# Performance work log

Hardware: AMD Instinct MI355X
Metric: run time of the kernel (lower is better)

## Reference

```python
import jax, jax.numpy as jnp
import numpy as np

WB = 8   # weight bit width (signed int8, power-of-two scale)
AB = 8   # activation bit width (uint8, power-of-two scale)
BB = 8   # bias bit width

# (name, c_in, c_out, kernel) for every QuantConv2d in order
_CFG = [("1", 3, 32, 3), ("2", 32, 16, 3), ("31", 16, 16, 1), ("32", 16, 32, 3),
        ("33", 32, 32, 1), ("34", 32, 64, 3), ("41", 64, 32, 1), ("42", 32, 64, 3),
        ("43", 64, 32, 1), ("44", 32, 64, 3), ("45", 64, 32, 1), ("46", 32, 64, 3)]
_POOL_AFTER = {"1", "2", "34"}  # MaxPool2d(2,2) follows these blocks


def _ste_round(x):
    # straight-through rounding (Brevitas-style fake quant)
    return x + jax.lax.stop_gradient(jnp.round(x) - x)


def _p2_scale(maxv, levels):
    # power-of-two (fixed point) per-tensor scale covering maxv with `levels` steps
    maxv = jnp.maximum(jax.lax.stop_gradient(maxv), 1e-8)
    return 2.0 ** jnp.ceil(jnp.log2(maxv / levels))


def quant_int(x, bw):
    # signed symmetric fixed-point fake quant (Int8WeightPerTensorFixedPoint style)
    n = 2.0 ** (bw - 1) - 1.0
    s = _p2_scale(jnp.max(jnp.abs(x)), n)
    return jnp.clip(_ste_round(x / s), -n - 1.0, n) * s


def quant_uint(x, bw):
    # unsigned fixed-point fake quant (Uint8ActPerTensorFixedPoint style)
    n = 2.0 ** bw - 1.0
    s = _p2_scale(jnp.max(x), n)
    return jnp.clip(_ste_round(x / s), 0.0, n) * s


def _conv(x, w, pad):
    return jax.lax.conv_general_dilated(
        x, w, window_strides=(1, 1), padding=[(pad, pad), (pad, pad)],
        dimension_numbers=("NCHW", "OIHW", "NCHW"))


def _maxpool2(x):
    return jax.lax.reduce_window(x, -jnp.inf, jax.lax.max,
                                 (1, 1, 2, 2), (1, 1, 2, 2), "VALID")


def _forward(x, p):
    # QuantIdentity on input (uint8 fixed point)
    x = quant_uint(x, AB)
    for n, ci, co, k in _CFG:
        pad = (k - 1) // 2
        y = _conv(x, quant_int(p["w" + n], WB), pad)               # quantized conv, no bias
        # BatchNorm2dToQuantScaleBias: per-channel affine with quantized scale/bias
        y = (y * quant_int(p["sg" + n], WB)[None, :, None, None]
             + quant_int(p["sb" + n], BB)[None, :, None, None])
        x = quant_uint(jax.nn.relu(y), AB)                          # QuantReLU
        if n in _POOL_AFTER:
            x = _maxpool2(x)
    # TruncAvgPool2d(28,28) over the remaining 28x28 map + RoundTo8bit requant
    x = quant_uint(jnp.mean(x, axis=(2, 3)), 8)                     # [B, 64]
    h = x @ quant_int(p["fw1"], WB).T + quant_int(p["fb1"], BB)     # linear51
    h = quant_uint(jax.nn.relu(h), AB)                              # relu5
    return h @ quant_int(p["fw2"], WB).T + quant_int(p["fb2"], BB)  # linear52


def setup_inputs() -> dict:
    key = jax.random.key(0)
    ks = iter(jax.random.split(key, 64))
    inp = {"x": jax.random.uniform(next(ks), (16, 3, 224, 224), jnp.float32)}
    for n, ci, co, k in _CFG:
        inp["w" + n] = jax.random.normal(next(ks), (co, ci, k, k), jnp.float32) * 0.1
        inp["sg" + n] = jax.random.uniform(next(ks), (co,), jnp.float32, 0.5, 1.5)
        inp["sb" + n] = jax.random.normal(next(ks), (co,), jnp.float32) * 0.1
    inp["fw1"] = jax.random.normal(next(ks), (16, 64), jnp.float32) * 0.1
    inp["fb1"] = jax.random.normal(next(ks), (16,), jnp.float32) * 0.1
    inp["fw2"] = jax.random.normal(next(ks), (10, 16), jnp.float32) * 0.1
    inp["fb2"] = jax.random.normal(next(ks), (10,), jnp.float32) * 0.1
    return inp


def reference(x, w1, sg1, sb1, w2, sg2, sb2, w31, sg31, sb31, w32, sg32, sb32,
              w33, sg33, sb33, w34, sg34, sb34, w41, sg41, sb41, w42, sg42, sb42,
              w43, sg43, sb43, w44, sg44, sb44, w45, sg45, sb45, w46, sg46, sb46,
              fw1, fb1, fw2, fb2):
    p = dict(locals())
    x = p.pop("x")
    return _forward(x, p)
```

## Files before the change

### kernel.cpp

```cpp
#include <hip/hip_runtime.h>
#include <math.h>

#define NL 12

typedef short v8s __attribute__((ext_vector_type(8)));
typedef float v4f __attribute__((ext_vector_type(4)));

struct PrepArgs {
  const float* in[40];
  void* out[40];
  int n[40];
  int mode[40];
  int tc[40];
  int ci[40], kk[40], kp[40], co[40];
};

__device__ inline float p2_scale_f(float maxv, float levels) {
  float r = __fdiv_rn(fmaxf(maxv, 1e-8f), levels);
  unsigned b = __float_as_uint(r);
  unsigned e = (b >> 23) & 0xffu;
  e += (b & 0x7fffffu) ? 1u : 0u;
  return __uint_as_float(e << 23);
}

__device__ inline float p2_inv(float s) {
  return __uint_as_float((254u << 23) - __float_as_uint(s));
}

__device__ inline float block_reduce_max256(float v) {
  __shared__ float sm[4];
  #pragma unroll
  for (int off = 32; off; off >>= 1) v = fmaxf(v, __shfl_down(v, off));
  if ((threadIdx.x & 63) == 0) sm[threadIdx.x >> 6] = v;
  __syncthreads();
  if (threadIdx.x == 0) v = fmaxf(fmaxf(sm[0], sm[1]), fmaxf(sm[2], sm[3]));
  return v;
}

__device__ inline void slot_max_update(float* slot, float v) {
  volatile unsigned int* su = (volatile unsigned int*)slot;
  unsigned int bits = __float_as_uint(v);
  if (bits > *su) atomicMax((unsigned int*)slot, bits);
}

__device__ inline short ibf16(float v) {
  return (short)(__float_as_uint(v) >> 16);
}

__global__ void prep_kernel(PrepArgs a, float* wslot,
                            const float* __restrict__ x, int nx, float* slot0) {
  if (blockIdx.x >= 40) {
    const float4* xv = (const float4*)x;
    const int nv = nx >> 2;
    float m0 = 0.f, m1 = 0.f, m2 = 0.f, m3 = 0.f;
    for (int i = (blockIdx.x - 40) * 256 + threadIdx.x; i < nv;
         i += (gridDim.x - 40) * 256) {
      float4 v = xv[i];
      m0 = fmaxf(m0, v.x); m1 = fmaxf(m1, v.y);
      m2 = fmaxf(m2, v.z); m3 = fmaxf(m3, v.w);
    }
    float m = fmaxf(fmaxf(m0, m1), fmaxf(m2, m3));
    float bm = block_reduce_max256(m);
    if (threadIdx.x == 0) slot_max_update(slot0, bm);
    return;
  }
  __shared__ float ssc;
  const int t = blockIdx.x;
  const float* in = a.in[t];
  const int n = a.n[t], mode = a.mode[t];
  float m = 0.f;
  if (mode == 2) {
    const float4* in4 = (const float4*)in;
    const int n4 = n >> 2;
    for (int i = threadIdx.x; i < n4; i += 256) {
      float4 v = in4[i];
      m = fmaxf(m, fmaxf(fmaxf(fabsf(v.x), fabsf(v.y)),
                         fmaxf(fabsf(v.z), fabsf(v.w))));
    }
  } else {
    for (int i = threadIdx.x; i < n; i += 256) m = fmaxf(m, fabsf(in[i]));
  }
  float bm = block_reduce_max256(m);
  if (threadIdx.x == 0) {
    ssc = p2_scale_f(bm, 127.0f);
    if (mode == 2) wslot[t] = ssc;
  }
  __syncthreads();
  const float s = ssc;
  if (mode == 2) {
    ushort* o = (ushort*)a.out[t];
    const int CI = a.ci[t], KK = a.kk[t], KP = a.kp[t], CO = a.co[t];
    const int KT = CI * KK;
    for (int i = threadIdx.x; i < CO * KP; i += 256) {
      int co = i / KP, k = i % KP;
      ushort v = 0;
      if (k < KT) {
        int khkw = k / CI, ci = k % CI;
        float q = rintf(__fdiv_rn(in[(co * CI + ci) * KK + khkw], s));
        q = fminf(fmaxf(q, -128.f), 127.f);
        v = (ushort)(__float_as_uint(q) >> 16);
      }
      o[i] = v;
    }
  } else {
    float* o = (float*)a.out[t];
    const int tc = a.tc[t];
    const int nw = (mode == 1) ? n / tc : 1;
    for (int i = threadIdx.x; i < n; i += 256) {
      float q = rintf(__fdiv_rn(in[i], s));
      q = fminf(fmaxf(q, -128.f), 127.f);
      float v = __fmul_rn(q, s);
      if (mode == 1) o[(i % nw) * tc + i / nw] = v;
      else o[i] = v;
    }
  }
}


template <int CI, int H, int CO, bool K3, bool POOL, int CSPLIT>
__global__ __launch_bounds__(256)
void conv_mfma(const float* __restrict__ in, const short* __restrict__ wt,
               const float* __restrict__ sg, const float* __restrict__ sb,
               float* __restrict__ out, const float* __restrict__ slot_in,
               const float* __restrict__ wslotp, float* slot_out) {
  constexpr int W = H;
  constexpr int KT = (K3 ? 9 : 1) * CI;
  constexpr int SLABS = (KT + 31) / 32;
  constexpr int KP = SLABS * 32;
  constexpr int COT = CO / (16 * CSPLIT);
  constexpr int HO = POOL ? H / 2 : H;
  constexpr int WO = POOL ? W / 2 : W;

  const int lane = threadIdx.x & 63, widx = threadIdx.x >> 6;
  const int quad = lane >> 4, col = lane & 15;
  const float s_in = p2_scale_f(slot_in[0], 255.0f);
  const float inv = p2_inv(s_in);
  const float S = __fmul_rn(s_in, wslotp[0]);
  const int wv = blockIdx.x * 4 + widx;
  const int mt = wv / CSPLIT, ct = wv % CSPLIT;

  int n, h, w, ph = 0, pw = 0;
  if constexpr (POOL) {
    constexpr int PB = (HO / 2) * (WO / 2);
    n = mt / PB; int r = mt % PB;
    ph = r / (WO / 2); pw = r % (WO / 2);
    h = 4 * ph + (col >> 2); w = 4 * pw + (col & 3);
  } else {
    int p = mt * 16 + col;
    n = p / (H * W); int r = p % (H * W);
    h = r / W; w = r % W;
  }
  const float* ibase = in + (size_t)n * H * W * CI;

  float4 fa[SLABS], fb[SLABS];
  bool vm[SLABS];
  #pragma unroll
  for (int slab = 0; slab < SLABS; slab++) {
    const int kbase = slab * 32 + quad * 8;
    const float* ap;
    if constexpr (K3) {
      const int khkw = min(kbase / CI, 8);
      const int cib = kbase % CI;
      const int kh = khkw / 3, kw = khkw - kh * 3;
      const int hh = h + kh - 1, ww = w + kw - 1;
      vm[slab] = (hh >= 0) && (hh < H) && (ww >= 0) && (ww < W);
      const int hc = min(max(hh, 0), H - 1), wc = min(max(ww, 0), W - 1);
      ap = ibase + (size_t)(hc * W + wc) * CI + cib;
    } else {
      vm[slab] = true;
      ap = ibase + (size_t)(h * W + w) * CI + (kbase % CI);
    }
    fa[slab] = ((const float4*)ap)[0];
    fb[slab] = ((const float4*)ap)[1];
  }

  v4f acc[COT];
  #pragma unroll
  for (int c = 0; c < COT; c++) acc[c] = (v4f){0.f, 0.f, 0.f, 0.f};

  #pragma unroll
  for (int slab = 0; slab < SLABS; slab++) {
    const int kbase = slab * 32 + quad * 8;
    float ff[8] = {fa[slab].x, fa[slab].y, fa[slab].z, fa[slab].w,
                   fb[slab].x, fb[slab].y, fb[slab].z, fb[slab].w};
    v8s a;
    #pragma unroll
    for (int j = 0; j < 8; j++) {
      float q = rintf(__fmul_rn(ff[j], inv));
      a[j] = vm[slab] ? ibf16(q) : (short)0;
    }
    #pragma unroll
    for (int c = 0; c < COT; c++) {
      v8s b = *(const v8s*)(wt + (size_t)((ct * COT + c) * 16 + col) * KP + kbase);
      acc[c] = __builtin_amdgcn_mfma_f32_16x16x32_bf16(a, b, acc[c], 0, 0, 0);
    }
  }

  float zmax = 0.f;
  #pragma unroll
  for (int c = 0; c < COT; c++) {
    const int cog = (ct * COT + c) * 16 + col;
    const float g = sg[cog], bb = sb[cog];
    float z[4];
    #pragma unroll
    for (int r2 = 0; r2 < 4; r2++) {
      float t = __fmul_rn(acc[c][r2], S);
      z[r2] = fmaxf(__fadd_rn(__fmul_rn(t, g), bb), 0.f);
    }
    if constexpr (POOL) {
      float h0 = fmaxf(z[0], z[1]), h1 = fmaxf(z[2], z[3]);
      float o0 = fmaxf(h0, __shfl_xor(h0, 16));
      float o1 = fmaxf(h1, __shfl_xor(h1, 16));
      zmax = fmaxf(zmax, fmaxf(o0, o1));
      if (!(quad & 1)) {
        int oh = 2 * ph + (quad >> 1), ow = 2 * pw;
        float* op = out + ((size_t)((n * HO + oh) * WO + ow)) * CO + cog;
        op[0] = o0; op[CO] = o1;
      }
    } else {
      const int pbase = mt * 16 + quad * 4;
      #pragma unroll
      for (int r2 = 0; r2 < 4; r2++) {
        out[(size_t)(pbase + r2) * CO + cog] = z[r2];
        zmax = fmaxf(zmax, z[r2]);
      }
    }
  }
  float bm = block_reduce_max256(zmax);
  if (threadIdx.x == 0) slot_max_update(slot_out, bm);
}

__global__ __launch_bounds__(256)
void conv1_mfma(const float* __restrict__ x, const short* __restrict__ wt,
                const float* __restrict__ sg, const float* __restrict__ sb,
                float* __restrict__ out, const float* __restrict__ slot_in,
                const float* __restrict__ wslotp, float* slot_out) {
  const int lane = threadIdx.x & 63, widx = threadIdx.x >> 6;
  const int quad = lane >> 4, col = lane & 15;
  const float s_in = p2_scale_f(slot_in[0], 255.0f);
  const float inv = p2_inv(s_in);
  const float S = __fmul_rn(s_in, wslotp[0]);
  const int wv = blockIdx.x * 4 + widx;
  const int n = wv / 3136, r = wv % 3136;
  const int ph = r / 56, pw = r % 56;
  const int h = 4 * ph + (col >> 2), w = 4 * pw + (col & 3);

  float fv[8];
  bool vm[8];
  #pragma unroll
  for (int j = 0; j < 8; j++) {
    int k = quad * 8 + j;
    int kc = min(k, 26);
    int khkw = kc / 3, ci = kc - khkw * 3;
    int kh = khkw / 3, kw = khkw - kh * 3;
    int hh = h + kh - 1, ww = w + kw - 1;
    vm[j] = (hh >= 0) && (hh < 224) && (ww >= 0) && (ww < 224);
    int hc = min(max(hh, 0), 223), wc = min(max(ww, 0), 223);
    fv[j] = x[((n * 3 + ci) * 224 + hc) * 224 + wc];
  }
  v8s a;
  #pragma unroll
  for (int j = 0; j < 8; j++) {
    float q = rintf(__fmul_rn(fv[j], inv));
    a[j] = vm[j] ? ibf16(q) : (short)0;
  }
  v4f acc[2];
  acc[0] = (v4f){0.f, 0.f, 0.f, 0.f};
  acc[1] = acc[0];
  #pragma unroll
  for (int c = 0; c < 2; c++) {
    v8s b = *(const v8s*)(wt + (size_t)(c * 16 + col) * 32 + quad * 8);
    acc[c] = __builtin_amdgcn_mfma_f32_16x16x32_bf16(a, b, acc[c], 0, 0, 0);
  }
  float zmax = 0.f;
  #pragma unroll
  for (int c = 0; c < 2; c++) {
    const int cog = c * 16 + col;
    const float g = sg[cog], bb = sb[cog];
    float z[4];
    #pragma unroll
    for (int r2 = 0; r2 < 4; r2++) {
      float t = __fmul_rn(acc[c][r2], S);
      z[r2] = fmaxf(__fadd_rn(__fmul_rn(t, g), bb), 0.f);
    }
    float h0 = fmaxf(z[0], z[1]), h1 = fmaxf(z[2], z[3]);
    float o0 = fmaxf(h0, __shfl_xor(h0, 16));
    float o1 = fmaxf(h1, __shfl_xor(h1, 16));
    zmax = fmaxf(zmax, fmaxf(o0, o1));
    if (!(quad & 1)) {
      int oh = 2 * ph + (quad >> 1), ow = 2 * pw;
      float* op = out + ((size_t)((n * 112 + oh) * 112 + ow)) * 32 + cog;
      op[0] = o0; op[32] = o1;
    }
  }
  float bm = block_reduce_max256(zmax);
  if (threadIdx.x == 0) slot_max_update(slot_out, bm);
}

__global__ void avgpool_kernel(const float* __restrict__ in, float* __restrict__ out,
                               const float* __restrict__ slot_in, float* slot_out) {
  __shared__ float red[1024];
  const float s = p2_scale_f(slot_in[0], 255.0f);
  const float inv = p2_inv(s);
  const int nn = blockIdx.x, co = threadIdx.x & 63, part = threadIdx.x >> 6;
  const float* p = in + (size_t)nn * 784 * 64;
  float sum = 0.f;
  for (int i = part * 49; i < part * 49 + 49; i++)
    sum += __fmul_rn(rintf(__fmul_rn(p[i * 64 + co], inv)), s);
  red[threadIdx.x] = sum;
  __syncthreads();
  if (threadIdx.x < 64) {
    float tot = 0.f;
    #pragma unroll
    for (int k2 = 0; k2 < 16; k2++) tot += red[k2 * 64 + co];
    float m = __fdiv_rn(tot, 784.0f);
    out[nn * 64 + co] = m;
    slot_max_update(slot_out, m);
  }
}

__global__ void tail_kernel(const float* __restrict__ pooled,
                            const float* __restrict__ fw1, const float* __restrict__ fb1,
                            const float* __restrict__ fw2, const float* __restrict__ fb2,
                            const float* __restrict__ slot_in, float* __restrict__ out) {
  __shared__ float xq[1024];
  __shared__ float hq[256];
  __shared__ float s2s;
  const int t = threadIdx.x;
  const float s = p2_scale_f(slot_in[0], 255.0f);
  const float inv = p2_inv(s);
  for (int i = t; i < 1024; i += 256)
    xq[i] = __fmul_rn(rintf(__fmul_rn(pooled[i], inv)), s);
  __syncthreads();
  const int n = t >> 4, j = t & 15;
  float acc = 0.f;
  #pragma unroll 8
  for (int k = 0; k < 64; k++) acc += xq[n * 64 + k] * fw1[k * 16 + j];
  float z = fmaxf(__fadd_rn(acc, fb1[j]), 0.f);
  float bm = block_reduce_max256(z);
  if (t == 0) s2s = p2_scale_f(bm, 255.0f);
  __syncthreads();
  const float s2 = s2s, inv2 = p2_inv(s2);
  hq[t] = __fmul_rn(rintf(__fmul_rn(z, inv2)), s2);
  __syncthreads();
  if (t < 160) {
    const int n2 = t / 10, j2 = t % 10;
    float a2 = 0.f;
    #pragma unroll
    for (int k = 0; k < 16; k++) a2 += hq[n2 * 16 + k] * fw2[k * 10 + j2];
    out[t] = __fadd_rn(a2, fb2[j2]);
  }
}

extern "C" void kernel_launch(void* const* d_in, const int* in_sizes, int n_in,
                              void* d_out, int out_size, void* d_ws, size_t ws_size,
                              hipStream_t stream) {
  static const int h_ci[NL] = {3, 32, 16, 16, 32, 32, 64, 32, 64, 32, 64, 32};
  static const int h_co[NL] = {32, 16, 16, 32, 32, 64, 32, 64, 32, 64, 32, 64};
  static const int h_kk[NL] = {9, 9, 1, 9, 1, 9, 1, 9, 1, 9, 1, 9};
  static const int h_kp[NL] = {32, 288, 32, 160, 32, 288, 64, 288, 64, 288, 64, 288};

  float* ws = (float*)d_ws;
  float* slots = ws;
  float* wslot = ws + 16;
  size_t off = 32;

  short* wq[NL];
  for (int l = 0; l < NL; l++) {
    wq[l] = (short*)(ws + off);
    off += (size_t)(h_co[l] * h_kp[l] + 1) / 2;
  }
  float* sgq[NL]; float* sbq[NL];
  for (int l = 0; l < NL; l++) { sgq[l] = ws + off; off += 64; }
  for (int l = 0; l < NL; l++) { sbq[l] = ws + off; off += 64; }
  float* fw1q = ws + off; off += 1024;
  float* fb1q = ws + off; off += 16;
  float* fw2q = ws + off; off += 160;
  float* fb2q = ws + off; off += 16;
  float* A = ws + off; off += 6422528;
  float* B = ws + off; off += 1605632;
  float* P = ws + off; off += 1024;

  PrepArgs pa;
  for (int l = 0; l < NL; l++) {
    pa.in[l] = (const float*)d_in[1 + 3 * l]; pa.out[l] = (void*)wq[l];
    pa.n[l] = h_co[l] * h_ci[l] * h_kk[l];
    pa.mode[l] = 2; pa.tc[l] = 0;
    pa.ci[l] = h_ci[l]; pa.kk[l] = h_kk[l]; pa.kp[l] = h_kp[l]; pa.co[l] = h_co[l];
    pa.in[12 + l] = (const float*)d_in[2 + 3 * l]; pa.out[12 + l] = (void*)sgq[l];
    pa.n[12 + l] = h_co[l]; pa.mode[12 + l] = 0; pa.tc[12 + l] = 0;
    pa.ci[12 + l] = pa.kk[12 + l] = pa.kp[12 + l] = pa.co[12 + l] = 0;
    pa.in[24 + l] = (const float*)d_in[3 + 3 * l]; pa.out[24 + l] = (void*)sbq[l];
    pa.n[24 + l] = h_co[l]; pa.mode[24 + l] = 0; pa.tc[24 + l] = 0;
    pa.ci[24 + l] = pa.kk[24 + l] = pa.kp[24 + l] = pa.co[24 + l] = 0;
  }
  pa.in[36] = (const float*)d_in[37]; pa.out[36] = (void*)fw1q;
  pa.n[36] = 1024; pa.mode[36] = 1; pa.tc[36] = 16;
  pa.ci[36] = pa.kk[36] = pa.kp[36] = pa.co[36] = 0;
  pa.in[37] = (const float*)d_in[38]; pa.out[37] = (void*)fb1q;
  pa.n[37] = 16; pa.mode[37] = 0; pa.tc[37] = 0;
  pa.ci[37] = pa.kk[37] = pa.kp[37] = pa.co[37] = 0;
  pa.in[38] = (const float*)d_in[39]; pa.out[38] = (void*)fw2q;
  pa.n[38] = 160; pa.mode[38] = 1; pa.tc[38] = 10;
  pa.ci[38] = pa.kk[38] = pa.kp[38] = pa.co[38] = 0;
  pa.in[39] = (const float*)d_in[40]; pa.out[39] = (void*)fb2q;
  pa.n[39] = 10; pa.mode[39] = 0; pa.tc[39] = 0;
  pa.ci[39] = pa.kk[39] = pa.kp[39] = pa.co[39] = 0;

  const float* x = (const float*)d_in[0];
  const int nx = 16 * 3 * 224 * 224;

  hipMemsetAsync(slots, 0, 16 * sizeof(float), stream);
  prep_kernel<<<40 + 294, 256, 0, stream>>>(pa, wslot, x, nx, slots + 0);

  conv1_mfma<<<12544, 256, 0, stream>>>(x, wq[0], sgq[0], sbq[0], A,
                                        slots + 0, wslot + 0, slots + 1);
  conv_mfma<32, 112, 16, true, true, 1><<<3136, 256, 0, stream>>>(
      A, wq[1], sgq[1], sbq[1], B, slots + 1, wslot + 1, slots + 2);
  conv_mfma<16, 56, 16, false, false, 1><<<784, 256, 0, stream>>>(
      B, wq[2], sgq[2], sbq[2], A, slots + 2, wslot + 2, slots + 3);
  conv_mfma<16, 56, 32, true, false, 2><<<1568, 256, 0, stream>>>(
      A, wq[3], sgq[3], sbq[3], B, slots + 3, wslot + 3, slots + 4);
  conv_mfma<32, 56, 32, false, false, 2><<<1568, 256, 0, stream>>>(
      B, wq[4], sgq[4], sbq[4], A, slots + 4, wslot + 4, slots + 5);
  conv_mfma<32, 56, 64, true, true, 2><<<1568, 256, 0, stream>>>(
      A, wq[5], sgq[5], sbq[5], B, slots + 5, wslot + 5, slots + 6);
  conv_mfma<64, 28, 32, false, false, 2><<<392, 256, 0, stream>>>(
      B, wq[6], sgq[6], sbq[6], A, slots + 6, wslot + 6, slots + 7);
  conv_mfma<32, 28, 64, true, false, 2><<<392, 256, 0, stream>>>(
      A, wq[7], sgq[7], sbq[7], B, slots + 7, wslot + 7, slots + 8);
  conv_mfma<64, 28, 32, false, false, 2><<<392, 256, 0, stream>>>(
      B, wq[8], sgq[8], sbq[8], A, slots + 8, wslot + 8, slots + 9);
  conv_mfma<32, 28, 64, true, false, 2><<<392, 256, 0, stream>>>(
      A, wq[9], sgq[9], sbq[9], B, slots + 9, wslot + 9, slots + 10);
  conv_mfma<64, 28, 32, false, false, 2><<<392, 256, 0, stream>>>(
      B, wq[10], sgq[10], sbq[10], A, slots + 10, wslot + 10, slots + 11);
  conv_mfma<32, 28, 64, true, false, 2><<<392, 256, 0, stream>>>(
      A, wq[11], sgq[11], sbq[11], B, slots + 11, wslot + 11, slots + 12);

  avgpool_kernel<<<16, 1024, 0, stream>>>(B, P, slots + 12, slots + 13);
  tail_kernel<<<1, 256, 0, stream>>>(P, fw1q, fb1q, fw2q, fb2q, slots + 13,
                                     (float*)d_out);
}
```

Measured before the change: 383.2 us.

## Pre-quantize input into channel-interleaved bf16 layout for conv1 tap loads

Adds a separate kernel that quantizes the input image once into an NHWC4 bf16 buffer. conv1 then loads one 8-byte vector per 3x3 tap instead of eight scattered fp32 loads from the three channel planes. The conv1 weights are repacked to 64-wide K so the taps map onto two MFMAs. This trades an extra pass over the input and an extra launch for cheaper, coalesced conv1 gathers and no per-element quantization in the conv.

```diff
diff --git a/kernel.cpp b/kernel.cpp
--- a/kernel.cpp
+++ b/kernel.cpp
@@ -69,7 +69,7 @@
   const float* in = a.in[t];
   const int n = a.n[t], mode = a.mode[t];
   float m = 0.f;
-  if (mode == 2) {
+  if (mode >= 2) {
     const float4* in4 = (const float4*)in;
     const int n4 = n >> 2;
     for (int i = threadIdx.x; i < n4; i += 256) {
@@ -83,11 +83,24 @@
   float bm = block_reduce_max256(m);
   if (threadIdx.x == 0) {
     ssc = p2_scale_f(bm, 127.0f);
-    if (mode == 2) wslot[t] = ssc;
+    if (mode >= 2) wslot[t] = ssc;
   }
   __syncthreads();
   const float s = ssc;
-  if (mode == 2) {
+  if (mode == 3) {
+    ushort* o = (ushort*)a.out[t];
+    for (int i = threadIdx.x; i < 32 * 64; i += 256) {
+      int co = i >> 6, k = i & 63;
+      int khkw = k >> 2, ci = k & 3;
+      ushort v = 0;
+      if (khkw < 9 && ci < 3) {
+        float q = rintf(__fdiv_rn(in[(co * 3 + ci) * 9 + khkw], s));
+        q = fminf(fmaxf(q, -128.f), 127.f);
+        v = (ushort)(__float_as_uint(q) >> 16);
+      }
+      o[i] = v;
+    }
+  } else if (mode == 2) {
     ushort* o = (ushort*)a.out[t];
     const int CI = a.ci[t], KK = a.kk[t], KP = a.kp[t], CO = a.co[t];
     const int KT = CI * KK;
@@ -114,6 +127,28 @@
       else o[i] = v;
     }
   }
+}
+
+__global__ void quantx_kernel(const float* __restrict__ x, ushort* __restrict__ xt,
+                              const float* __restrict__ slot_in) {
+  const float s = p2_scale_f(slot_in[0], 255.0f);
+  const float inv = p2_inv(s);
+  const int nh = blockIdx.x;
+  const int w = threadIdx.x;
+  if (w >= 224) return;
+  const int n = nh / 224;
+  const float* base = x + (size_t)n * 3 * 224 * 224 + (size_t)(nh % 224) * 224
+                      + (size_t)(n == n ? 0 : 0);
+  const float* b0 = x + ((size_t)(n * 3 + 0) * 224 + (nh % 224)) * 224;
+  const float* b1 = x + ((size_t)(n * 3 + 1) * 224 + (nh % 224)) * 224;
+  const float* b2 = x + ((size_t)(n * 3 + 2) * 224 + (nh % 224)) * 224;
+  (void)base;
+  ushort4 o;
+  o.x = (ushort)ibf16(rintf(__fmul_rn(b0[w], inv)));
+  o.y = (ushort)ibf16(rintf(__fmul_rn(b1[w], inv)));
+  o.z = (ushort)ibf16(rintf(__fmul_rn(b2[w], inv)));
+  o.w = 0;
+  ((ushort4*)xt)[(size_t)nh * 224 + w] = o;
 }
 
 
@@ -231,46 +266,48 @@
 }
 
 __global__ __launch_bounds__(256)
-void conv1_mfma(const float* __restrict__ x, const short* __restrict__ wt,
+void conv1_mfma(const ushort* __restrict__ xt, const short* __restrict__ wt,
                 const float* __restrict__ sg, const float* __restrict__ sb,
                 float* __restrict__ out, const float* __restrict__ slot_in,
                 const float* __restrict__ wslotp, float* slot_out) {
   const int lane = threadIdx.x & 63, widx = threadIdx.x >> 6;
   const int quad = lane >> 4, col = lane & 15;
   const float s_in = p2_scale_f(slot_in[0], 255.0f);
-  const float inv = p2_inv(s_in);
   const float S = __fmul_rn(s_in, wslotp[0]);
   const int wv = blockIdx.x * 4 + widx;
   const int n = wv / 3136, r = wv % 3136;
   const int ph = r / 56, pw = r % 56;
   const int h = 4 * ph + (col >> 2), w = 4 * pw + (col & 3);
-
-  float fv[8];
-  bool vm[8];
-  #pragma unroll
-  for (int j = 0; j < 8; j++) {
-    int k = quad * 8 + j;
-    int kc = min(k, 26);
-    int khkw = kc / 3, ci = kc - khkw * 3;
-    int kh = khkw / 3, kw = khkw - kh * 3;
+  const ushort* ibase = xt + (size_t)n * 224 * 224 * 4;
+
+  auto loadtap = [&](int t) -> ushort4 {
+    int kh = t / 3, kw = t - kh * 3;
     int hh = h + kh - 1, ww = w + kw - 1;
-    vm[j] = (hh >= 0) && (hh < 224) && (ww >= 0) && (ww < 224);
+    bool valid = (hh >= 0) && (hh < 224) && (ww >= 0) && (ww < 224);
     int hc = min(max(hh, 0), 223), wc = min(max(ww, 0), 223);
-    fv[j] = x[((n * 3 + ci) * 224 + hc) * 224 + wc];
-  }
-  v8s a;
-  #pragma unroll
-  for (int j = 0; j < 8; j++) {
-    float q = rintf(__fmul_rn(fv[j], inv));
-    a[j] = vm[j] ? ibf16(q) : (short)0;
-  }
+    ushort4 v = *(const ushort4*)(ibase + ((size_t)(hc * 224 + wc) << 2));
+    if (!valid) v = (ushort4){0, 0, 0, 0};
+    return v;
+  };
+  ushort4 cA = loadtap(2 * quad);
+  ushort4 cB = loadtap(2 * quad + 1);
+  ushort4 cC = loadtap(8);
+
+  v8s a0, a1;
+  a0[0] = (short)cA.x; a0[1] = (short)cA.y; a0[2] = (short)cA.z; a0[3] = (short)cA.w;
+  a0[4] = (short)cB.x; a0[5] = (short)cB.y; a0[6] = (short)cB.z; a0[7] = (short)cB.w;
+  a1[0] = (short)cC.x; a1[1] = (short)cC.y; a1[2] = (short)cC.z; a1[3] = (short)cC.w;
+  a1[4] = 0; a1[5] = 0; a1[6] = 0; a1[7] = 0;
+
   v4f acc[2];
   acc[0] = (v4f){0.f, 0.f, 0.f, 0.f};
   acc[1] = acc[0];
   #pragma unroll
   for (int c = 0; c < 2; c++) {
-    v8s b = *(const v8s*)(wt + (size_t)(c * 16 + col) * 32 + quad * 8);
-    acc[c] = __builtin_amdgcn_mfma_f32_16x16x32_bf16(a, b, acc[c], 0, 0, 0);
+    v8s b0 = *(const v8s*)(wt + (size_t)(c * 16 + col) * 64 + quad * 8);
+    v8s b1 = *(const v8s*)(wt + (size_t)(c * 16 + col) * 64 + 32 + quad * 8);
+    acc[c] = __builtin_amdgcn_mfma_f32_16x16x32_bf16(a0, b0, acc[c], 0, 0, 0);
+    acc[c] = __builtin_amdgcn_mfma_f32_16x16x32_bf16(a1, b1, acc[c], 0, 0, 0);
   }
   float zmax = 0.f;
   #pragma unroll
@@ -358,7 +395,7 @@
   static const int h_ci[NL] = {3, 32, 16, 16, 32, 32, 64, 32, 64, 32, 64, 32};
   static const int h_co[NL] = {32, 16, 16, 32, 32, 64, 32, 64, 32, 64, 32, 64};
   static const int h_kk[NL] = {9, 9, 1, 9, 1, 9, 1, 9, 1, 9, 1, 9};
-  static const int h_kp[NL] = {32, 288, 32, 160, 32, 288, 64, 288, 64, 288, 64, 288};
+  static const int h_kp[NL] = {64, 288, 32, 160, 32, 288, 64, 288, 64, 288, 64, 288};
 
   float* ws = (float*)d_ws;
   float* slots = ws;
@@ -377,6 +414,8 @@
   float* fb1q = ws + off; off += 16;
   float* fw2q = ws + off; off += 160;
   float* fb2q = ws + off; off += 16;
+  off = (off + 1) & ~(size_t)1;
+  ushort* XT = (ushort*)(ws + off); off += 1605632;
   float* A = ws + off; off += 6422528;
   float* B = ws + off; off += 1605632;
   float* P = ws + off; off += 1024;
@@ -385,7 +424,7 @@
   for (int l = 0; l < NL; l++) {
     pa.in[l] = (const float*)d_in[1 + 3 * l]; pa.out[l] = (void*)wq[l];
     pa.n[l] = h_co[l] * h_ci[l] * h_kk[l];
-    pa.mode[l] = 2; pa.tc[l] = 0;
+    pa.mode[l] = (l == 0) ? 3 : 2; pa.tc[l] = 0;
     pa.ci[l] = h_ci[l]; pa.kk[l] = h_kk[l]; pa.kp[l] = h_kp[l]; pa.co[l] = h_co[l];
     pa.in[12 + l] = (const float*)d_in[2 + 3 * l]; pa.out[12 + l] = (void*)sgq[l];
     pa.n[12 + l] = h_co[l]; pa.mode[12 + l] = 0; pa.tc[12 + l] = 0;
@@ -412,8 +451,9 @@
 
   hipMemsetAsync(slots, 0, 16 * sizeof(float), stream);
   prep_kernel<<<40 + 294, 256, 0, stream>>>(pa, wslot, x, nx, slots + 0);
-
-  conv1_mfma<<<12544, 256, 0, stream>>>(x, wq[0], sgq[0], sbq[0], A,
+  quantx_kernel<<<16 * 224, 256, 0, stream>>>(x, XT, slots + 0);
+
+  conv1_mfma<<<12544, 256, 0, stream>>>(XT, wq[0], sgq[0], sbq[0], A,
                                         slots + 0, wslot + 0, slots + 1);
   conv_mfma<32, 112, 16, true, true, 1><<<3136, 256, 0, stream>>>(
       A, wq[1], sgq[1], sbq[1], B, slots + 1, wslot + 1, slots + 2);
```

New measurement: 415.7 us. +8.5%, slower.
